# Kernel tuning notes

Measured on AMD Instinct MI355X. Metric: run time of the kernel, lower is better.

Reference implementation:

```python
import jax, jax.numpy as jnp
import numpy as np

N = 65536      # total points (single batch, multiple of patch_size)
C = 512        # channels
H = 8          # heads
K = 256        # patch (window) size
SCALE = 0.125  # head_dim ** -0.5


def setup_inputs() -> dict:
    key = jax.random.key(0)
    k1, k2, k3, k4 = jax.random.split(key, 4)
    feat = jax.random.normal(k1, (N, C), dtype=jnp.float32)
    # serialized order = permutation of points; inverse undoes it
    order = jax.random.permutation(k2, N).astype(jnp.int64)
    inverse = jnp.argsort(order).astype(jnp.int64)
    Wqkv = jax.random.normal(k3, (C, 3 * C), dtype=jnp.float32) * (C ** -0.5)
    bqkv = jnp.zeros((3 * C,), dtype=jnp.float32)
    Wproj = jax.random.normal(k4, (C, C), dtype=jnp.float32) * (C ** -0.5)
    bproj = jnp.zeros((C,), dtype=jnp.float32)
    return {"feat": feat, "order": order, "inverse": inverse,
            "Wqkv": Wqkv, "bqkv": bqkv, "Wproj": Wproj, "bproj": bproj}


def reference(feat, order, inverse, Wqkv, bqkv, Wproj, bproj):
    d = C // H
    P = N // K  # number of windows
    # QKV projection then gather into serialized patch order
    qkv = feat @ Wqkv + bqkv                    # [N, 3C]
    qkv = qkv[order].reshape(P, K, 3, H, d)     # [P, K, 3, H, d]
    q, k, v = qkv[:, :, 0], qkv[:, :, 1], qkv[:, :, 2]  # each [P, K, H, d]
    # windowed attention within each patch
    scores = jnp.einsum("pkhd,pmhd->phkm", q, k) * SCALE  # [P, H, K, K]
    attn = jax.nn.softmax(scores, axis=-1)
    out = jnp.einsum("phkm,pmhd->pkhd", attn, v)          # [P, K, H, d]
    out = out.reshape(N, C)[inverse]                       # unpad / de-serialize
    return out @ Wproj + bproj
```

## Files before the change

kernel.cpp:

```cpp
#include <hip/hip_runtime.h>
#include <stdint.h>

#define N_TOK 65536
#define CDIM  512
#define C3    1536
#define HEADS 8
#define DHEAD 64
#define KTOK  256
#define PGRP  256

typedef __attribute__((ext_vector_type(8))) short bf16x8;
typedef __attribute__((ext_vector_type(4))) float f32x4;

__device__ __forceinline__ unsigned short f2bf(float f) {
  union { float f; unsigned u; } t; t.f = f;
  return (unsigned short)((t.u + 0x7fffu + ((t.u >> 16) & 1u)) >> 16);
}

__global__ __launch_bounds__(256) void cvt_f32_bf16(const float* __restrict__ in,
                                                    unsigned short* __restrict__ out) {
  size_t i = ((size_t)blockIdx.x * 256 + threadIdx.x) * 4;
  float4 v = *(const float4*)(in + i);
  ushort4 o;
  o.x = f2bf(v.x); o.y = f2bf(v.y); o.z = f2bf(v.z); o.w = f2bf(v.w);
  *(ushort4*)(out + i) = o;
}

__global__ __launch_bounds__(256) void transpose_cvt(const float* __restrict__ in,
                                                     unsigned short* __restrict__ out,
                                                     int R, int Cc) {
  __shared__ float tile[32][33];
  int c0 = blockIdx.x * 32, r0 = blockIdx.y * 32;
  int tx = threadIdx.x & 31, ty = threadIdx.x >> 5;
  for (int i = ty; i < 32; i += 8)
    tile[i][tx] = in[(size_t)(r0 + i) * Cc + c0 + tx];
  __syncthreads();
  for (int i = ty; i < 32; i += 8)
    out[(size_t)(c0 + i) * R + r0 + tx] = f2bf(tile[tx][i]);
}

template <int OF32>
__global__ __launch_bounds__(512, 2) void gemm256(const unsigned short* __restrict__ A,
                                                  const unsigned short* __restrict__ Bt,
                                                  const float* __restrict__ bias,
                                                  void* __restrict__ Cout,
                                                  const int* __restrict__ gather,
                                                  int Nn, int Kk, int nbn) {
  __shared__ __align__(16) unsigned short As[2][256 * 64];
  __shared__ __align__(16) unsigned short Bs[2][256 * 64];

  int cpx = gridDim.x >> 3;
  int wk = (blockIdx.x & 7) * cpx + (blockIdx.x >> 3);
  int bm = wk / nbn, bn = wk % nbn;
  int m0 = bm * 256, n0 = bn * 256;

  int tid = threadIdx.x;
  int wv = tid >> 6, ln = tid & 63, g = ln >> 4, c = ln & 15;
  int wr = wv >> 2, wc = wv & 3;
  int NT = Kk >> 6;

  const char* Ab = (const char*)A;
  const char* Bb = (const char*)Bt;
  int lr = tid >> 3;
  int cg = (tid & 7) ^ (lr & 7);
  unsigned aoff[2][2], boff[2][2];
#pragma unroll
  for (int h2 = 0; h2 < 2; ++h2)
#pragma unroll
    for (int j = 0; j < 2; ++j) {
      int row = h2 * 128 + j * 64 + lr;
      int ga = gather ? gather[m0 + row] : (m0 + row);
      aoff[h2][j] = (unsigned)(((size_t)ga * Kk + cg * 8) * 2);
      boff[h2][j] = (unsigned)(((size_t)(n0 + row) * Kk + cg * 8) * 2);
    }

#define STAGE_A(t, h2) do { int _s = (t) & 1; unsigned _k = (unsigned)(t) * 128u;             \
    __builtin_amdgcn_global_load_lds(                                                          \
        (__attribute__((address_space(1))) void*)(void*)(Ab + aoff[h2][0] + _k),               \
        (__attribute__((address_space(3))) void*)&As[_s][((h2) * 1024 + wv * 64) * 8],         \
        16, 0, 0);                                                                             \
    __builtin_amdgcn_global_load_lds(                                                          \
        (__attribute__((address_space(1))) void*)(void*)(Ab + aoff[h2][1] + _k),               \
        (__attribute__((address_space(3))) void*)&As[_s][((h2) * 1024 + 512 + wv * 64) * 8],   \
        16, 0, 0);                                                                             \
  } while (0)
#define STAGE_B(t, h2) do { int _s = (t) & 1; unsigned _k = (unsigned)(t) * 128u;             \
    __builtin_amdgcn_global_load_lds(                                                          \
        (__attribute__((address_space(1))) void*)(void*)(Bb + boff[h2][0] + _k),               \
        (__attribute__((address_space(3))) void*)&Bs[_s][((h2) * 1024 + wv * 64) * 8],         \
        16, 0, 0);                                                                             \
    __builtin_amdgcn_global_load_lds(                                                          \
        (__attribute__((address_space(1))) void*)(void*)(Bb + boff[h2][1] + _k),               \
        (__attribute__((address_space(3))) void*)&Bs[_s][((h2) * 1024 + 512 + wv * 64) * 8],   \
        16, 0, 0);                                                                             \
  } while (0)
#define RD_A(mi, kc) (*(const bf16x8*)&Ac[((((2 * (mi) + wr) * 16 + c) * 8 + (((kc) * 4 + g) ^ (c & 7))) * 8)])
#define RD_B(ni, kc) (*(const bf16x8*)&Bc[((((4 * (ni) + wc) * 16 + c) * 8 + (((kc) * 4 + g) ^ (c & 7))) * 8)])

  f32x4 acc[8][4];
#pragma unroll
  for (int mi = 0; mi < 8; ++mi)
#pragma unroll
    for (int ni = 0; ni < 4; ++ni)
      acc[mi][ni] = (f32x4){0.f, 0.f, 0.f, 0.f};

  STAGE_A(0, 0); STAGE_A(0, 1); STAGE_B(0, 0); STAGE_B(0, 1);
  STAGE_A(1, 0); STAGE_A(1, 1); STAGE_B(1, 0); STAGE_B(1, 1);
  asm volatile("s_waitcnt vmcnt(8)" ::: "memory");
  __builtin_amdgcn_s_barrier();

  bf16x8 af[4][2], bf[2][2];

#pragma unroll 1
  for (int v = 0; v < NT; ++v) {
    unsigned short* Ac = &As[v & 1][0];
    unsigned short* Bc = &Bs[v & 1][0];

#pragma unroll
    for (int i = 0; i < 4; ++i)
#pragma unroll
      for (int kc = 0; kc < 2; ++kc) af[i][kc] = RD_A(i, kc);
#pragma unroll
    for (int j = 0; j < 2; ++j)
#pragma unroll
      for (int kc = 0; kc < 2; ++kc) bf[j][kc] = RD_B(j, kc);
    if (v >= 1 && v + 1 < NT) STAGE_A(v + 1, 1);
    __builtin_amdgcn_s_barrier();
    asm volatile("s_waitcnt lgkmcnt(0)" ::: "memory");
    __builtin_amdgcn_sched_barrier(0);
    __builtin_amdgcn_s_setprio(1);
#pragma unroll
    for (int i = 0; i < 4; ++i)
#pragma unroll
      for (int j = 0; j < 2; ++j) {
        acc[i][j] = __builtin_amdgcn_mfma_f32_16x16x32_bf16(af[i][0], bf[j][0], acc[i][j], 0, 0, 0);
        acc[i][j] = __builtin_amdgcn_mfma_f32_16x16x32_bf16(af[i][1], bf[j][1], acc[i][j], 0, 0, 0);
      }
    __builtin_amdgcn_s_setprio(0);
    __builtin_amdgcn_s_barrier();

#pragma unroll
    for (int j = 0; j < 2; ++j)
#pragma unroll
      for (int kc = 0; kc < 2; ++kc) bf[j][kc] = RD_B(2 + j, kc);
    if (v >= 1 && v + 1 < NT) STAGE_B(v + 1, 0);
    __builtin_amdgcn_s_barrier();
    asm volatile("s_waitcnt lgkmcnt(0)" ::: "memory");
    __builtin_amdgcn_sched_barrier(0);
    __builtin_amdgcn_s_setprio(1);
#pragma unroll
    for (int i = 0; i < 4; ++i)
#pragma unroll
      for (int j = 0; j < 2; ++j) {
        acc[i][2 + j] = __builtin_amdgcn_mfma_f32_16x16x32_bf16(af[i][0], bf[j][0], acc[i][2 + j], 0, 0, 0);
        acc[i][2 + j] = __builtin_amdgcn_mfma_f32_16x16x32_bf16(af[i][1], bf[j][1], acc[i][2 + j], 0, 0, 0);
      }
    __builtin_amdgcn_s_setprio(0);
    __builtin_amdgcn_s_barrier();

#pragma unroll
    for (int i = 0; i < 4; ++i)
#pragma unroll
      for (int kc = 0; kc < 2; ++kc) af[i][kc] = RD_A(4 + i, kc);
    if (v + 2 < NT) STAGE_A(v + 2, 0);
    __builtin_amdgcn_s_barrier();
    asm volatile("s_waitcnt lgkmcnt(0)" ::: "memory");
    __builtin_amdgcn_sched_barrier(0);
    __builtin_amdgcn_s_setprio(1);
#pragma unroll
    for (int i = 0; i < 4; ++i)
#pragma unroll
      for (int j = 0; j < 2; ++j) {
        acc[4 + i][2 + j] = __builtin_amdgcn_mfma_f32_16x16x32_bf16(af[i][0], bf[j][0], acc[4 + i][2 + j], 0, 0, 0);
        acc[4 + i][2 + j] = __builtin_amdgcn_mfma_f32_16x16x32_bf16(af[i][1], bf[j][1], acc[4 + i][2 + j], 0, 0, 0);
      }
    __builtin_amdgcn_s_setprio(0);
    __builtin_amdgcn_s_barrier();

#pragma unroll
    for (int j = 0; j < 2; ++j)
#pragma unroll
      for (int kc = 0; kc < 2; ++kc) bf[j][kc] = RD_B(j, kc);
    if (v + 2 < NT) STAGE_B(v + 2, 1);
    __builtin_amdgcn_s_barrier();
    asm volatile("s_waitcnt lgkmcnt(0)" ::: "memory");
    __builtin_amdgcn_sched_barrier(0);
    __builtin_amdgcn_s_setprio(1);
#pragma unroll
    for (int i = 0; i < 4; ++i)
#pragma unroll
      for (int j = 0; j < 2; ++j) {
        acc[4 + i][j] = __builtin_amdgcn_mfma_f32_16x16x32_bf16(af[i][0], bf[j][0], acc[4 + i][j], 0, 0, 0);
        acc[4 + i][j] = __builtin_amdgcn_mfma_f32_16x16x32_bf16(af[i][1], bf[j][1], acc[4 + i][j], 0, 0, 0);
      }
    __builtin_amdgcn_s_setprio(0);
    if (v + 2 < NT) asm volatile("s_waitcnt vmcnt(4)" ::: "memory");
    else            asm volatile("s_waitcnt vmcnt(0)" ::: "memory");
    __builtin_amdgcn_s_barrier();
  }

#pragma unroll
  for (int ni = 0; ni < 4; ++ni) {
    int col = n0 + (4 * ni + wc) * 16 + c;
    float bv = bias[col];
#pragma unroll
    for (int mi = 0; mi < 8; ++mi) {
      int rowb = m0 + (2 * mi + wr) * 16 + g * 4;
#pragma unroll
      for (int rr = 0; rr < 4; ++rr) {
        float vv = acc[mi][ni][rr] + bv;
        if (OF32) ((float*)Cout)[(size_t)(rowb + rr) * Nn + col] = vv;
        else ((unsigned short*)Cout)[(size_t)(rowb + rr) * Nn + col] = f2bf(vv);
      }
    }
  }
#undef STAGE_A
#undef STAGE_B
#undef RD_A
#undef RD_B
}

__global__ __launch_bounds__(256, 2) void attn_k(const unsigned short* __restrict__ qkv,
                                                 const int* __restrict__ order,
                                                 unsigned short* __restrict__ attnout) {
  __shared__ __align__(16) unsigned short Ks[KTOK * 64];
  __shared__ __align__(16) unsigned short Vt[64 * 256];
  __shared__ __align__(16) unsigned short Pt[4][2][16 * 64];

  int p = blockIdx.x >> 3, h = blockIdx.x & 7;
  int tid = threadIdx.x;
  int wv = tid >> 6, ln = tid & 63, g = ln >> 4, c = ln & 15;

  const unsigned short* base = qkv + (size_t)p * KTOK * C3 + h * DHEAD;

  {
    const unsigned short* krow = base + CDIM + (size_t)tid * C3;
#pragma unroll
    for (int j = 0; j < 8; ++j) {
      bf16x8 kv = *(const bf16x8*)(krow + j * 8);
      *(bf16x8*)&Ks[(tid * 8 + (j ^ (tid & 7))) * 8] = kv;
    }
    const unsigned short* vrow = base + 2 * CDIM + (size_t)tid * C3;
#pragma unroll
    for (int j = 0; j < 8; ++j) {
      bf16x8 vvv = *(const bf16x8*)(vrow + j * 8);
#pragma unroll
      for (int e = 0; e < 8; ++e) {
        int d = j * 8 + e;
        Vt[d * 256 + (((tid >> 3) ^ (d & 7)) << 3) + (tid & 7)] = (unsigned short)vvv[e];
      }
    }
  }
  __syncthreads();

#pragma unroll 1
  for (int t = 0; t < 4; ++t) {
    int q0 = wv * 64 + t * 16;
    const unsigned short* qrow = base + (size_t)(q0 + c) * C3;
    bf16x8 aq0 = *(const bf16x8*)(qrow + g * 8);
    bf16x8 aq1 = *(const bf16x8*)(qrow + 32 + g * 8);

    f32x4 s[16];
#pragma unroll
    for (int mt = 0; mt < 16; ++mt) {
      int m = mt * 16 + c;
      bf16x8 bk0 = *(const bf16x8*)&Ks[(m * 8 + ((0 + g) ^ (m & 7))) * 8];
      bf16x8 bk1 = *(const bf16x8*)&Ks[(m * 8 + ((4 + g) ^ (m & 7))) * 8];
      f32x4 z = (f32x4){0.f, 0.f, 0.f, 0.f};
      z = __builtin_amdgcn_mfma_f32_16x16x32_bf16(aq0, bk0, z, 0, 0, 0);
      s[mt] = __builtin_amdgcn_mfma_f32_16x16x32_bf16(aq1, bk1, z, 0, 0, 0);
    }

    float mx[4], sm[4];
#pragma unroll
    for (int rr = 0; rr < 4; ++rr) {
      float m1 = s[0][rr];
#pragma unroll
      for (int mt = 1; mt < 16; ++mt) m1 = fmaxf(m1, s[mt][rr]);
#pragma unroll
      for (int off = 1; off < 16; off <<= 1) m1 = fmaxf(m1, __shfl_xor(m1, off, 64));
      mx[rr] = m1;
    }
#pragma unroll
    for (int rr = 0; rr < 4; ++rr) sm[rr] = 0.f;
#pragma unroll
    for (int mt = 0; mt < 16; ++mt)
#pragma unroll
      for (int rr = 0; rr < 4; ++rr) {
        float e = __expf((s[mt][rr] - mx[rr]) * 0.125f);
        s[mt][rr] = e;
        sm[rr] += e;
      }
#pragma unroll
    for (int rr = 0; rr < 4; ++rr) {
      float t2 = sm[rr];
#pragma unroll
      for (int off = 1; off < 16; off <<= 1) t2 += __shfl_xor(t2, off, 64);
      sm[rr] = 1.f / t2;
    }

    f32x4 o[4];
#pragma unroll
    for (int dt = 0; dt < 4; ++dt) o[dt] = (f32x4){0.f, 0.f, 0.f, 0.f};
#pragma unroll
    for (int ch = 0; ch < 4; ++ch) {
      unsigned short* pt = &Pt[wv][ch & 1][0];
#pragma unroll
      for (int mtl = 0; mtl < 4; ++mtl) {
        int mt = ch * 4 + mtl;
        int mcol = mtl * 16 + c;
#pragma unroll
        for (int rr = 0; rr < 4; ++rr) {
          int q = g * 4 + rr;
          pt[q * 64 + (((mcol >> 3) ^ (q & 7)) << 3) + (mcol & 7)] =
              f2bf(s[mt][rr] * sm[rr]);
        }
      }
#pragma unroll
      for (int mcl = 0; mcl < 2; ++mcl) {
        int cg = mcl * 4 + g;
        bf16x8 ap = *(const bf16x8*)&pt[(c * 8 + (cg ^ (c & 7))) * 8];
        int cgm = (ch * 2 + mcl) * 4 + g;
#pragma unroll
        for (int dt = 0; dt < 4; ++dt) {
          int d = dt * 16 + c;
          bf16x8 bv = *(const bf16x8*)&Vt[(d * 32 + (cgm ^ (d & 7))) * 8];
          o[dt] = __builtin_amdgcn_mfma_f32_16x16x32_bf16(ap, bv, o[dt], 0, 0, 0);
        }
      }
    }

#pragma unroll
    for (int rr = 0; rr < 4; ++rr) {
      int orow = order[p * KTOK + q0 + g * 4 + rr];
      size_t rb = (size_t)orow * CDIM + h * DHEAD;
#pragma unroll
      for (int dt = 0; dt < 4; ++dt)
        attnout[rb + dt * 16 + c] = f2bf(o[dt][rr]);
    }
  }
}

extern "C" void kernel_launch(void* const* d_in, const int* in_sizes, int n_in,
                              void* d_out, int out_size, void* d_ws, size_t ws_size,
                              hipStream_t stream) {
  const float* feat  = (const float*)d_in[0];
  const int*   order = (const int*)d_in[1];
  const float* Wqkv  = (const float*)d_in[3];
  const float* bqkv  = (const float*)d_in[4];
  const float* Wproj = (const float*)d_in[5];
  const float* bproj = (const float*)d_in[6];
  float* out = (float*)d_out;

  char* ws = (char*)d_ws;
  unsigned short* qkv    = (unsigned short*)ws;
  unsigned short* featb  = (unsigned short*)(ws + (size_t)N_TOK * C3 * 2);
  unsigned short* attn   = featb;
  unsigned short* wqkvT  = (unsigned short*)(ws + (size_t)N_TOK * C3 * 2 + (size_t)N_TOK * CDIM * 2);
  unsigned short* wprojT = wqkvT + C3 * CDIM;

  cvt_f32_bf16<<<(N_TOK * CDIM) / (256 * 4), 256, 0, stream>>>(feat, featb);
  transpose_cvt<<<dim3(C3 / 32, CDIM / 32), 256, 0, stream>>>(Wqkv, wqkvT, CDIM, C3);
  transpose_cvt<<<dim3(CDIM / 32, CDIM / 32), 256, 0, stream>>>(Wproj, wprojT, CDIM, CDIM);

  gemm256<0><<<(N_TOK / 256) * (C3 / 256), 512, 0, stream>>>(
      featb, wqkvT, bqkv, qkv, order, C3, CDIM, C3 / 256);

  attn_k<<<PGRP * HEADS, 256, 0, stream>>>(qkv, order, attn);

  gemm256<1><<<(N_TOK / 256) * (CDIM / 256), 512, 0, stream>>>(
      attn, wprojT, bproj, out, nullptr, CDIM, CDIM, CDIM / 256);
}
```

Baseline: 576.4 us.

## Rewrite window attention with 32x32 MFMA, register-resident P, and async K loads

The attention kernel moves from 16x16x32 to 32x32x16 bf16 MFMA tiles. It computes S transposed (K times Q) so the softmax row reductions become mostly in-lane, with a single cross-half shuffle. The softmax probabilities are packed with v_cvt_pk_bf16 and rearranged through permlane32_swap into PV operands, which removes the per-wave LDS staging buffer Pt and its writes and reads. K is loaded straight into LDS with global_load_lds, Q fragments are prefetched, and s_setprio is raised around the MFMA bursts. The trade-off is higher register pressure from the 16-wide accumulators, which could lower occupancy below the 2-blocks launch bound.

```diff
diff --git a/kernel.cpp b/kernel.cpp
--- a/kernel.cpp
+++ b/kernel.cpp
@@ -11,10 +11,18 @@
 
 typedef __attribute__((ext_vector_type(8))) short bf16x8;
 typedef __attribute__((ext_vector_type(4))) float f32x4;
+typedef __attribute__((ext_vector_type(16))) float f32x16;
+typedef __attribute__((ext_vector_type(4))) unsigned u32x4;
 
 __device__ __forceinline__ unsigned short f2bf(float f) {
   union { float f; unsigned u; } t; t.f = f;
   return (unsigned short)((t.u + 0x7fffu + ((t.u >> 16) & 1u)) >> 16);
+}
+
+__device__ __forceinline__ unsigned cvt_pk_bf16(float lo, float hi) {
+  unsigned r;
+  asm("v_cvt_pk_bf16_f32 %0, %1, %2" : "=v"(r) : "v"(lo), "v"(hi));
+  return r;
 }
 
 __global__ __launch_bounds__(256) void cvt_f32_bf16(const float* __restrict__ in,
@@ -225,118 +233,130 @@
                                                  unsigned short* __restrict__ attnout) {
   __shared__ __align__(16) unsigned short Ks[KTOK * 64];
   __shared__ __align__(16) unsigned short Vt[64 * 256];
-  __shared__ __align__(16) unsigned short Pt[4][2][16 * 64];
 
   int p = blockIdx.x >> 3, h = blockIdx.x & 7;
   int tid = threadIdx.x;
-  int wv = tid >> 6, ln = tid & 63, g = ln >> 4, c = ln & 15;
+  int wv = tid >> 6, ln = tid & 63;
+  int lq = ln & 31;
+  int hl = ln >> 5;
 
   const unsigned short* base = qkv + (size_t)p * KTOK * C3 + h * DHEAD;
 
   {
-    const unsigned short* krow = base + CDIM + (size_t)tid * C3;
-#pragma unroll
-    for (int j = 0; j < 8; ++j) {
-      bf16x8 kv = *(const bf16x8*)(krow + j * 8);
-      *(bf16x8*)&Ks[(tid * 8 + (j ^ (tid & 7))) * 8] = kv;
-    }
+    int mlo = tid >> 3;
+    int j = (tid & 7) ^ (mlo & 7);
+    const unsigned short* ksrc = base + CDIM + j * 8;
+#pragma unroll
+    for (int i = 0; i < 8; ++i) {
+      int m = i * 32 + mlo;
+      __builtin_amdgcn_global_load_lds(
+          (const __attribute__((address_space(1))) void*)(ksrc + (size_t)m * C3),
+          (__attribute__((address_space(3))) void*)&Ks[((i << 8) + tid) * 8],
+          16, 0, 0);
+    }
+  }
+  {
     const unsigned short* vrow = base + 2 * CDIM + (size_t)tid * C3;
-#pragma unroll
-    for (int j = 0; j < 8; ++j) {
-      bf16x8 vvv = *(const bf16x8*)(vrow + j * 8);
+    bf16x8 vv[8];
+#pragma unroll
+    for (int j = 0; j < 8; ++j) vv[j] = *(const bf16x8*)(vrow + j * 8);
+#pragma unroll
+    for (int j = 0; j < 8; ++j)
 #pragma unroll
       for (int e = 0; e < 8; ++e) {
         int d = j * 8 + e;
-        Vt[d * 256 + (((tid >> 3) ^ (d & 7)) << 3) + (tid & 7)] = (unsigned short)vvv[e];
-      }
-    }
+        Vt[d * 256 + (((tid >> 3) ^ (d & 7)) << 3) + (tid & 7)] = (unsigned short)vv[j][e];
+      }
+  }
+
+  bf16x8 qfa[2][4];
+  {
+    const unsigned short* qr = base + (size_t)(wv * 64 + lq) * C3;
+#pragma unroll
+    for (int dk = 0; dk < 4; ++dk) qfa[0][dk] = *(const bf16x8*)(qr + dk * 16 + hl * 8);
   }
   __syncthreads();
 
-#pragma unroll 1
-  for (int t = 0; t < 4; ++t) {
-    int q0 = wv * 64 + t * 16;
-    const unsigned short* qrow = base + (size_t)(q0 + c) * C3;
-    bf16x8 aq0 = *(const bf16x8*)(qrow + g * 8);
-    bf16x8 aq1 = *(const bf16x8*)(qrow + 32 + g * 8);
-
-    f32x4 s[16];
-#pragma unroll
-    for (int mt = 0; mt < 16; ++mt) {
-      int m = mt * 16 + c;
-      bf16x8 bk0 = *(const bf16x8*)&Ks[(m * 8 + ((0 + g) ^ (m & 7))) * 8];
-      bf16x8 bk1 = *(const bf16x8*)&Ks[(m * 8 + ((4 + g) ^ (m & 7))) * 8];
-      f32x4 z = (f32x4){0.f, 0.f, 0.f, 0.f};
-      z = __builtin_amdgcn_mfma_f32_16x16x32_bf16(aq0, bk0, z, 0, 0, 0);
-      s[mt] = __builtin_amdgcn_mfma_f32_16x16x32_bf16(aq1, bk1, z, 0, 0, 0);
-    }
-
-    float mx[4], sm[4];
-#pragma unroll
-    for (int rr = 0; rr < 4; ++rr) {
-      float m1 = s[0][rr];
-#pragma unroll
-      for (int mt = 1; mt < 16; ++mt) m1 = fmaxf(m1, s[mt][rr]);
-#pragma unroll
-      for (int off = 1; off < 16; off <<= 1) m1 = fmaxf(m1, __shfl_xor(m1, off, 64));
-      mx[rr] = m1;
-    }
-#pragma unroll
-    for (int rr = 0; rr < 4; ++rr) sm[rr] = 0.f;
-#pragma unroll
-    for (int mt = 0; mt < 16; ++mt)
-#pragma unroll
-      for (int rr = 0; rr < 4; ++rr) {
-        float e = __expf((s[mt][rr] - mx[rr]) * 0.125f);
-        s[mt][rr] = e;
-        sm[rr] += e;
-      }
-#pragma unroll
-    for (int rr = 0; rr < 4; ++rr) {
-      float t2 = sm[rr];
-#pragma unroll
-      for (int off = 1; off < 16; off <<= 1) t2 += __shfl_xor(t2, off, 64);
-      sm[rr] = 1.f / t2;
-    }
-
-    f32x4 o[4];
-#pragma unroll
-    for (int dt = 0; dt < 4; ++dt) o[dt] = (f32x4){0.f, 0.f, 0.f, 0.f};
-#pragma unroll
-    for (int ch = 0; ch < 4; ++ch) {
-      unsigned short* pt = &Pt[wv][ch & 1][0];
-#pragma unroll
-      for (int mtl = 0; mtl < 4; ++mtl) {
-        int mt = ch * 4 + mtl;
-        int mcol = mtl * 16 + c;
-#pragma unroll
-        for (int rr = 0; rr < 4; ++rr) {
-          int q = g * 4 + rr;
-          pt[q * 64 + (((mcol >> 3) ^ (q & 7)) << 3) + (mcol & 7)] =
-              f2bf(s[mt][rr] * sm[rr]);
-        }
-      }
-#pragma unroll
-      for (int mcl = 0; mcl < 2; ++mcl) {
-        int cg = mcl * 4 + g;
-        bf16x8 ap = *(const bf16x8*)&pt[(c * 8 + (cg ^ (c & 7))) * 8];
-        int cgm = (ch * 2 + mcl) * 4 + g;
-#pragma unroll
-        for (int dt = 0; dt < 4; ++dt) {
-          int d = dt * 16 + c;
-          bf16x8 bv = *(const bf16x8*)&Vt[(d * 32 + (cgm ^ (d & 7))) * 8];
-          o[dt] = __builtin_amdgcn_mfma_f32_16x16x32_bf16(ap, bv, o[dt], 0, 0, 0);
-        }
-      }
-    }
-
-#pragma unroll
-    for (int rr = 0; rr < 4; ++rr) {
-      int orow = order[p * KTOK + q0 + g * 4 + rr];
-      size_t rb = (size_t)orow * CDIM + h * DHEAD;
-#pragma unroll
-      for (int dt = 0; dt < 4; ++dt)
-        attnout[rb + dt * 16 + c] = f2bf(o[dt][rr]);
+#pragma unroll
+  for (int t = 0; t < 2; ++t) {
+    int q0 = wv * 64 + t * 32;
+    int ordv[16];
+#pragma unroll
+    for (int r = 0; r < 16; ++r)
+      ordv[r] = order[p * KTOK + q0 + (r & 3) + 8 * (r >> 2) + 4 * hl];
+
+    f32x16 sa[8];
+    __builtin_amdgcn_s_setprio(1);
+#pragma unroll
+    for (int mt = 0; mt < 8; ++mt) {
+      f32x16 z;
+#pragma unroll
+      for (int r = 0; r < 16; ++r) z[r] = 0.f;
+      int m = mt * 32 + lq;
+#pragma unroll
+      for (int dk = 0; dk < 4; ++dk) {
+        bf16x8 kf = *(const bf16x8*)&Ks[(m * 8 + ((dk * 2 + hl) ^ (m & 7))) * 8];
+        z = __builtin_amdgcn_mfma_f32_32x32x16_bf16(kf, qfa[t][dk], z, 0, 0, 0);
+      }
+      sa[mt] = z;
+    }
+    __builtin_amdgcn_s_setprio(0);
+
+    if (t == 0) {
+      const unsigned short* qr = base + (size_t)(wv * 64 + 32 + lq) * C3;
+#pragma unroll
+      for (int dk = 0; dk < 4; ++dk) qfa[1][dk] = *(const bf16x8*)(qr + dk * 16 + hl * 8);
+    }
+
+    float mx = sa[0][0];
+#pragma unroll
+    for (int mt = 0; mt < 8; ++mt)
+#pragma unroll
+      for (int r = 0; r < 16; ++r) mx = fmaxf(mx, sa[mt][r]);
+    mx = fmaxf(mx, __shfl_xor(mx, 32, 64));
+    float sum = 0.f;
+#pragma unroll
+    for (int mt = 0; mt < 8; ++mt)
+#pragma unroll
+      for (int r = 0; r < 16; ++r) {
+        float e = __expf((sa[mt][r] - mx) * 0.125f);
+        sa[mt][r] = e;
+        sum += e;
+      }
+    sum += __shfl_xor(sum, 32, 64);
+    float inv = 1.f / sum;
+
+    f32x16 oa[2];
+#pragma unroll
+    for (int r = 0; r < 16; ++r) { oa[0][r] = 0.f; oa[1][r] = 0.f; }
+#pragma unroll
+    for (int kt = 0; kt < 16; ++kt) {
+      int mt = kt >> 1, rb = (kt & 1) * 8;
+      unsigned L0 = cvt_pk_bf16(sa[mt][rb + 0] * inv, sa[mt][rb + 1] * inv);
+      unsigned L1 = cvt_pk_bf16(sa[mt][rb + 2] * inv, sa[mt][rb + 3] * inv);
+      unsigned H0 = cvt_pk_bf16(sa[mt][rb + 4] * inv, sa[mt][rb + 5] * inv);
+      unsigned H1 = cvt_pk_bf16(sa[mt][rb + 6] * inv, sa[mt][rb + 7] * inv);
+      auto s0 = __builtin_amdgcn_permlane32_swap(L0, H0, false, false);
+      auto s1 = __builtin_amdgcn_permlane32_swap(L1, H1, false, false);
+      u32x4 pw;
+      pw[0] = s0[0]; pw[1] = s1[0]; pw[2] = s0[1]; pw[3] = s1[1];
+      bf16x8 pf = __builtin_bit_cast(bf16x8, pw);
+      __builtin_amdgcn_s_setprio(1);
+#pragma unroll
+      for (int dt = 0; dt < 2; ++dt) {
+        int d = dt * 32 + lq;
+        bf16x8 vf = *(const bf16x8*)&Vt[(d * 32 + ((kt * 2 + hl) ^ (d & 7))) * 8];
+        oa[dt] = __builtin_amdgcn_mfma_f32_32x32x16_bf16(pf, vf, oa[dt], 0, 0, 0);
+      }
+      __builtin_amdgcn_s_setprio(0);
+    }
+
+    size_t cb = (size_t)h * DHEAD + lq;
+#pragma unroll
+    for (int r = 0; r < 16; ++r) {
+      size_t rb2 = (size_t)ordv[r] * CDIM + cb;
+      attnout[rb2] = f2bf(oa[0][r]);
+      attnout[rb2 + 32] = f2bf(oa[1][r]);
     }
   }
 }
```

New measurement: 496.7 us. 13.8% less time.
